# Kernel optimization log

Hardware: AMD Instinct MI355X
Metric: run time of the kernel (lower is better)

The kernel has to match this reference:

```python
import jax, jax.numpy as jnp
import numpy as np

D, T, B = 128, 64, 512
EPS = 1e-5


def setup_inputs() -> dict:
    key = jax.random.key(0)
    k1, k2, k3, k4, k5 = jax.random.split(key, 5)
    inp = jax.random.normal(k1, (D, T, B), jnp.float32) * 0.1
    returns_partition = jax.random.normal(k2, (D, T, B), jnp.float32) * 0.01
    target = jax.random.normal(k3, (D,), jnp.float32) * 0.1
    hidden = jnp.zeros((D, 1, B), jnp.float32)  # forward arg (overwritten at t=0)
    # diagonally-dominant weight so the per-row denominators v[j,j] stay away from 0
    W = jnp.eye(D, dtype=jnp.float32) + 0.1 * jax.random.normal(k4, (D, D), jnp.float32)
    b = 0.1 * jax.random.normal(k5, (D,), jnp.float32)
    return {"input": inp, "target": target, "returns_partition": returns_partition,
            "hidden": hidden, "W": W, "b": b}


def _recurrence(h, v, absb, pi_bar):
    # h, pi_bar: [D, B]; v: [D, D] (row-normalized); absb: [D]
    d = h.shape[0]
    vd = jnp.diagonal(v)                                  # v[j, j], torch.matmul(vj, e_j)
    s = v @ (h - pi_bar)                                  # [D, B], s[j] = vj . (h - pi_bar)
    lam_p = (absb[:, None] - s) / vd[:, None]
    lam_m = (-absb[:, None] - s) / vd[:, None]
    delta = (jnp.where(s > absb[:, None], lam_p, 0.0)
             + jnp.where(s < -absb[:, None], lam_m, 0.0))  # [D, B]
    # hidden_new_j = h + delta[j] * e_j  =>  v @ (hidden_new_j - pi_bar) = s + v[:, j] (x) delta[j]
    snew = s[None, :, :] + v.T[:, :, None] * delta[:, None, :]      # [J, D, B]
    inside = (snew < absb[None, :, None] + EPS) & (snew > -absb[None, :, None] - EPS)
    # torch: judge_mat[j] = min over rows; then max over j  == any_j(all_k(...))
    judge_mat = jnp.any(jnp.all(inside, axis=1), axis=0).astype(h.dtype)  # [B]

    # sequential per-coordinate projection (order matters: row j uses updated state)
    def body(ht, j):
        sj = v[j] @ (ht - pi_bar)                          # [B]
        lp = (absb[j] - sj) / v[j, j]
        lm = (-absb[j] - sj) / v[j, j]
        dj = jnp.where(sj > absb[j], lp, 0.0) + jnp.where(sj < -absb[j], lm, 0.0)
        return ht.at[j].add(dj), None
    h_temp, _ = jax.lax.scan(body, h, jnp.arange(d))

    # 10-step bisection between pi_bar (feasible) and (1 - judge_mat) * h
    def bis(carry, _):
        h_in, h_out = carry
        h_m = h_in + (h_out - h_in) * 0.5
        sm = v @ (h_m - pi_bar)
        j = jnp.all((sm <= absb[:, None] + EPS) & (sm >= -absb[:, None] - EPS), axis=0)  # [B]
        return (jnp.where(j, h_m, h_in), jnp.where(j, h_out, h_m)), h_m
    h_out0 = (1.0 - judge_mat) * h
    _, h_ms = jax.lax.scan(bis, (pi_bar, h_out0), None, length=10)
    h_m = h_ms[-1]
    return judge_mat * h_temp + (1.0 - judge_mat) * h_m


def reference(input, target, returns_partition, hidden, W, b):
    d, t, bsz = input.shape
    norm = jnp.linalg.norm(W, axis=1, keepdims=True)
    v = W / jnp.maximum(norm, 1e-12)                      # F.normalize(W, p=2, dim=1)
    absb = jnp.abs(b)
    pi_bar = jnp.broadcast_to(target[:, None], (d, bsz))  # [D, B]

    h0 = input[:, 0, :]                                   # t = 0: hidden := input slice
    rs = jnp.moveaxis(returns_partition[:, :t - 1, :], 1, 0)  # [T-1, D, B]

    def step(h, r):
        adj = h * (1.0 + r) / (1.0 + jnp.sum(h * r, axis=0))
        hn = _recurrence(adj, v, absb, pi_bar)
        return hn, hn

    h_last, hs = jax.lax.scan(step, h0, rs)
    output = jnp.concatenate([h0[:, None, :], jnp.moveaxis(hs, 0, 1)], axis=1)  # [D, T, B]
    return output, h_last[:, None, :]
```

## Files before the change

kernel.cpp:

```cpp
#include <hip/hip_runtime.h>
#include <cstdint>

#define D 128
#define T 64
#define B 512
#define EPSF 1e-5f

__device__ __forceinline__ float lane_bcast(float x, int l) {
    return __int_as_float(__builtin_amdgcn_readlane(__float_as_int(x), l));
}

__device__ __forceinline__ float2 colpair(const float* csh, int j, int i2) {
    int f2 = j * 64 + (i2 ^ ((j & 7) << 1));
    return *(const float2*)(csh + 2 * f2);
}

__global__ __launch_bounds__(64) void prep_kernel(const float* __restrict__ W,
                                                  const float* __restrict__ b,
                                                  float* __restrict__ csw,
                                                  float* __restrict__ vd,
                                                  float* __restrict__ absb) {
    const int i = blockIdx.x;
    const int l = threadIdx.x;
    float w0 = W[i * D + l];
    float w1 = W[i * D + l + 64];
    float p = w0 * w0 + w1 * w1;
#pragma unroll
    for (int off = 32; off; off >>= 1) p += __shfl_xor(p, off);
    float norm = sqrtf(p);
    float scale = norm > 1e-12f ? norm : 1e-12f;
    float v0 = w0 / scale;
    float v1 = w1 / scale;
    const int i2 = i & 63, half = i >> 6;
    const int sw = (l & 7) << 1;
    csw[2 * (l * 64 + (i2 ^ sw)) + half] = v0;
    csw[2 * ((l + 64) * 64 + (i2 ^ sw)) + half] = v1;
    if (i < 64) { if (l == i) vd[i] = v0; }
    else        { if (l == i - 64) vd[i] = v1; }
    if (i == 0) {
        absb[l] = fabsf(b[l]);
        absb[l + 64] = fabsf(b[l + 64]);
    }
}

__global__ __launch_bounds__(128, 1) void rnn_kernel(const float* __restrict__ input,
                                                     const float* __restrict__ target,
                                                     const float* __restrict__ returns,
                                                     const float* __restrict__ W,
                                                     const float* __restrict__ cswg,
                                                     const float* __restrict__ vdg,
                                                     const float* __restrict__ absbg,
                                                     float* __restrict__ out) {
    __shared__ float csh[D * D];
    __shared__ float s_sh[2][2 * 64];
    __shared__ float ae_sh[2 * 64];

    const int tid = threadIdx.x;
    const int w = tid >> 6;
    const int lane = tid & 63;
    const int b = blockIdx.x * 2 + w;
    const int rlo = lane, rhi = lane + 64;

    {
        const float4* src = (const float4*)cswg;
        float4* dst = (float4*)csh;
#pragma unroll
        for (int c = 0; c < 32; ++c) dst[c * 128 + tid] = src[c * 128 + tid];
    }

    const float tgt_lo = target[rlo], tgt_hi = target[rhi];
    const float a_lo = absbg[rlo], a_hi = absbg[rhi];
    const float aeps_lo = a_lo + EPSF, aeps_hi = a_hi + EPSF;
    const float vd_lo = vdg[rlo], vd_hi = vdg[rhi];
    const float rvd_lo = 1.0f / vd_lo, rvd_hi = 1.0f / vd_hi;

    if (w == 0) *(float2*)&ae_sh[2 * lane] = make_float2(aeps_lo, aeps_hi);

    float4 va4[32], vb4[32];
    {
        const float4* wa = (const float4*)(W + rlo * D);
        const float4* wb = (const float4*)(W + rhi * D);
        float na0 = 0, na1 = 0, na2 = 0, na3 = 0;
        float nb0 = 0, nb1 = 0, nb2 = 0, nb3 = 0;
#pragma unroll
        for (int c = 0; c < 32; ++c) {
            float4 A = wa[c], Bv = wb[c];
            va4[c] = A; vb4[c] = Bv;
            na0 = fmaf(A.x, A.x, na0); na1 = fmaf(A.y, A.y, na1);
            na2 = fmaf(A.z, A.z, na2); na3 = fmaf(A.w, A.w, na3);
            nb0 = fmaf(Bv.x, Bv.x, nb0); nb1 = fmaf(Bv.y, Bv.y, nb1);
            nb2 = fmaf(Bv.z, Bv.z, nb2); nb3 = fmaf(Bv.w, Bv.w, nb3);
        }
        float nna = sqrtf((na0 + na1) + (na2 + na3));
        float nnb = sqrtf((nb0 + nb1) + (nb2 + nb3));
        float ra = 1.0f / (nna > 1e-12f ? nna : 1e-12f);
        float rb = 1.0f / (nnb > 1e-12f ? nnb : 1e-12f);
#pragma unroll
        for (int c = 0; c < 32; ++c) {
            va4[c].x *= ra; va4[c].y *= ra; va4[c].z *= ra; va4[c].w *= ra;
            vb4[c].x *= rb; vb4[c].y *= rb; vb4[c].z *= rb; vb4[c].w *= rb;
        }
    }
    __syncthreads();

    const float* va = (const float*)va4;
    const float* vb = (const float*)vb4;

    float h_lo = input[rlo * T * B + b];
    float h_hi = input[rhi * T * B + b];
    out[rlo * T * B + b] = h_lo;
    out[rhi * T * B + b] = h_hi;

    float r_lo = returns[rlo * T * B + b];
    float r_hi = returns[rhi * T * B + b];

    for (int t = 1; t < T; ++t) {
        float num_lo = h_lo * (1.0f + r_lo);
        float num_hi = h_hi * (1.0f + r_hi);
        float p = h_lo * r_lo + h_hi * r_hi;
#pragma unroll
        for (int off = 32; off; off >>= 1) p += __shfl_xor(p, off);
        float den = 1.0f + p;
        float adj_lo = num_lo / den;
        float adj_hi = num_hi / den;

        if (t < T - 1) {
            r_lo = returns[rlo * T * B + t * B + b];
            r_hi = returns[rhi * T * B + t * B + b];
        }

        const float x_lo = adj_lo - tgt_lo;
        const float x_hi = adj_hi - tgt_hi;

        float a0 = 0, a1 = 0, a2 = 0, a3 = 0;
        float b0 = 0, b1 = 0, b2 = 0, b3 = 0;
#pragma unroll
        for (int k = 0; k < 128; ++k) {
            float xk = (k < 64) ? lane_bcast(x_lo, k) : lane_bcast(x_hi, k - 64);
            switch (k & 3) {
                case 0: a0 = fmaf(va[k], xk, a0); b0 = fmaf(vb[k], xk, b0); break;
                case 1: a1 = fmaf(va[k], xk, a1); b1 = fmaf(vb[k], xk, b1); break;
                case 2: a2 = fmaf(va[k], xk, a2); b2 = fmaf(vb[k], xk, b2); break;
                default: a3 = fmaf(va[k], xk, a3); b3 = fmaf(vb[k], xk, b3); break;
            }
        }
        float s_lo = (a0 + a1) + (a2 + a3);
        float s_hi = (b0 + b1) + (b2 + b3);

        h_lo = adj_lo;
        h_hi = adj_hi;

        bool viol_lo = (s_lo > a_lo) || (s_lo < -a_lo);
        bool viol_hi = (s_hi > a_hi) || (s_hi < -a_hi);
        uint64_t mlo = __ballot(viol_lo);
        uint64_t mhi = __ballot(viol_hi);

        if ((mlo | mhi) != 0ull) {
            float dl = 0.0f, dh = 0.0f;
            if (s_lo > a_lo) dl = (a_lo - s_lo) / vd_lo;
            else if (s_lo < -a_lo) dl = (-a_lo - s_lo) / vd_lo;
            if (s_hi > a_hi) dh = (a_hi - s_hi) / vd_hi;
            else if (s_hi < -a_hi) dh = (-a_hi - s_hi) / vd_hi;

            int V = __popcll(mlo) + __popcll(mhi);
            bool judge = false;

            if (V <= 8) {
                bool in_lo = (s_lo < aeps_lo) && (s_lo > -aeps_lo);
                bool in_hi = (s_hi < aeps_hi) && (s_hi > -aeps_hi);
                judge = (__ballot(in_lo && in_hi) == ~0ull);
                if (!judge) {
                    uint64_t tml = mlo, tmh = mhi;
                    int jn[8];
                    float djs[8];
                    float2 cps[8];
#pragma unroll
                    for (int q = 0; q < 8; ++q) {
                        int j = -1;
                        if (tml) {
                            j = (int)__ffsll((unsigned long long)tml) - 1;
                            tml &= tml - 1;
                        } else if (tmh) {
                            j = 64 + (int)__ffsll((unsigned long long)tmh) - 1;
                            tmh &= tmh - 1;
                        }
                        jn[q] = j;
                        if (j >= 0) {
                            djs[q] = lane_bcast((j < 64) ? dl : dh, j & 63);
                            cps[q] = colpair(csh, j, lane);
                        }
                    }
#pragma unroll
                    for (int q = 0; q < 8; ++q) {
                        if (jn[q] >= 0 && !judge) {
                            float n_lo = fmaf(cps[q].x, djs[q], s_lo);
                            float n_hi = fmaf(cps[q].y, djs[q], s_hi);
                            bool pl = (n_lo < aeps_lo) && (n_lo > -aeps_lo);
                            bool ph = (n_hi < aeps_hi) && (n_hi > -aeps_hi);
                            if (__ballot(pl && ph) == ~0ull) judge = true;
                        }
                    }
                }
            } else {
                *(float2*)&s_sh[w][2 * lane] = make_float2(s_lo, s_hi);
                float m1 = -1.0f, m2 = -1.0f;
#pragma unroll
                for (int c = 0; c < 32; ++c) {
                    int f4 = lane * 32 + (c ^ (lane & 7));
                    float4 c1 = *(const float4*)(csh + 4 * f4);
                    float4 c2 = *(const float4*)(csh + 4 * f4 + 8192);
                    float4 sv = *(const float4*)&s_sh[w][4 * c];
                    float4 ae = *(const float4*)&ae_sh[4 * c];
                    m1 = fmaxf(m1, fabsf(fmaf(c1.x, dl, sv.x)) - ae.x);
                    m1 = fmaxf(m1, fabsf(fmaf(c1.y, dl, sv.y)) - ae.y);
                    m1 = fmaxf(m1, fabsf(fmaf(c1.z, dl, sv.z)) - ae.z);
                    m1 = fmaxf(m1, fabsf(fmaf(c1.w, dl, sv.w)) - ae.w);
                    m2 = fmaxf(m2, fabsf(fmaf(c2.x, dh, sv.x)) - ae.x);
                    m2 = fmaxf(m2, fabsf(fmaf(c2.y, dh, sv.y)) - ae.y);
                    m2 = fmaxf(m2, fabsf(fmaf(c2.z, dh, sv.z)) - ae.z);
                    m2 = fmaxf(m2, fabsf(fmaf(c2.w, dh, sv.w)) - ae.w);
                }
                judge = ((__ballot(m1 < 0.0f) | __ballot(m2 < 0.0f)) != 0ull);
            }

            if (judge) {
                uint64_t rem_lo = ~0ull, rem_hi = ~0ull;
                while (true) {
                    uint64_t m1b = __ballot((s_lo > a_lo) || (s_lo < -a_lo)) & rem_lo;
                    uint64_t m2b = __ballot((s_hi > a_hi) || (s_hi < -a_hi)) & rem_hi;
                    int j;
                    if (m1b) {
                        int jl = (int)__ffsll((unsigned long long)m1b) - 1;
                        j = jl;
                        rem_lo = (jl == 63) ? 0ull : (~0ull << (jl + 1));
                    } else if (m2b) {
                        int jh = (int)__ffsll((unsigned long long)m2b) - 1;
                        j = 64 + jh;
                        rem_lo = 0ull;
                        rem_hi = (jh == 63) ? 0ull : (~0ull << (jh + 1));
                    } else {
                        break;
                    }
                    float dl2 = (s_lo > a_lo) ? (a_lo - s_lo) * rvd_lo
                               : ((s_lo < -a_lo) ? (-a_lo - s_lo) * rvd_lo : 0.0f);
                    float dh2 = (s_hi > a_hi) ? (a_hi - s_hi) * rvd_hi
                               : ((s_hi < -a_hi) ? (-a_hi - s_hi) * rvd_hi : 0.0f);
                    float srcv = (j < 64) ? dl2 : dh2;
                    float dj = lane_bcast(srcv, j & 63);
                    if (lane == (j & 63)) {
                        if (j < 64) h_lo += dj; else h_hi += dj;
                    }
                    float2 cp = colpair(csh, j, lane);
                    s_lo = fmaf(cp.x, dj, s_lo);
                    s_hi = fmaf(cp.y, dj, s_hi);
                }
            } else {
                float hin_lo = tgt_lo, hin_hi = tgt_hi;
                float sin_lo = 0.0f, sin_hi = 0.0f;
                float hout_lo = h_lo, hout_hi = h_hi;
                float sout_lo = s_lo, sout_hi = s_hi;
                float hm_lo = 0.0f, hm_hi = 0.0f;
#pragma unroll
                for (int it = 0; it < 10; ++it) {
                    hm_lo = hin_lo + (hout_lo - hin_lo) * 0.5f;
                    hm_hi = hin_hi + (hout_hi - hin_hi) * 0.5f;
                    float sm_lo = sin_lo + (sout_lo - sin_lo) * 0.5f;
                    float sm_hi = sin_hi + (sout_hi - sin_hi) * 0.5f;
                    bool pl = (sm_lo <= aeps_lo) && (sm_lo >= -aeps_lo);
                    bool ph = (sm_hi <= aeps_hi) && (sm_hi >= -aeps_hi);
                    bool inside = (__ballot(pl && ph) == ~0ull);
                    if (inside) {
                        hin_lo = hm_lo; hin_hi = hm_hi;
                        sin_lo = sm_lo; sin_hi = sm_hi;
                    } else {
                        hout_lo = hm_lo; hout_hi = hm_hi;
                        sout_lo = sm_lo; sout_hi = sm_hi;
                    }
                }
                h_lo = hm_lo;
                h_hi = hm_hi;
            }
        }

        out[rlo * T * B + t * B + b] = h_lo;
        out[rhi * T * B + t * B + b] = h_hi;
    }

    out[D * T * B + rlo * B + b] = h_lo;
    out[D * T * B + rhi * B + b] = h_hi;
}

extern "C" void kernel_launch(void* const* d_in, const int* in_sizes, int n_in,
                              void* d_out, int out_size, void* d_ws, size_t ws_size,
                              hipStream_t stream) {
    const float* input   = (const float*)d_in[0];
    const float* target  = (const float*)d_in[1];
    const float* returns = (const float*)d_in[2];
    const float* W = (const float*)d_in[4];
    const float* b = (const float*)d_in[5];
    float* out = (float*)d_out;

    float* csw  = (float*)d_ws;
    float* vd   = csw + D * D;
    float* absb = vd + D;

    prep_kernel<<<D, 64, 0, stream>>>(W, b, csw, vd, absb);
    rnn_kernel<<<B / 2, 128, 0, stream>>>(input, target, returns, W, csw, vd, absb, out);
}
```

Measured before the change: 239.5 us.

## Read weight columns from LDS instead of registers and batch projection lookahead

The per-thread register copy of the normalized weight rows (256 floats per thread) is dropped, and the mat-vec now streams swizzled column pairs from shared memory. The launch-bounds minimum-occupancy hint is removed, so register pressure falls and occupancy can rise. The sequential projection loop now prefetches up to four violating column pairs per pass and validates each against the live violation mask, aborting the batch when order changes. The swizzle indexing for the s/eps vectors in the judge check is also adjusted. In exchange, every mat-vec step pays an extra LDS read, and the projection loop gains branching complexity.

```diff
diff --git a/kernel.cpp b/kernel.cpp
--- a/kernel.cpp
+++ b/kernel.cpp
@@ -43,14 +43,13 @@
     }
 }
 
-__global__ __launch_bounds__(128, 1) void rnn_kernel(const float* __restrict__ input,
-                                                     const float* __restrict__ target,
-                                                     const float* __restrict__ returns,
-                                                     const float* __restrict__ W,
-                                                     const float* __restrict__ cswg,
-                                                     const float* __restrict__ vdg,
-                                                     const float* __restrict__ absbg,
-                                                     float* __restrict__ out) {
+__global__ __launch_bounds__(128) void rnn_kernel(const float* __restrict__ input,
+                                                  const float* __restrict__ target,
+                                                  const float* __restrict__ returns,
+                                                  const float* __restrict__ cswg,
+                                                  const float* __restrict__ vdg,
+                                                  const float* __restrict__ absbg,
+                                                  float* __restrict__ out) {
     __shared__ float csh[D * D];
     __shared__ float s_sh[2][2 * 64];
     __shared__ float ae_sh[2 * 64];
@@ -75,36 +74,12 @@
     const float rvd_lo = 1.0f / vd_lo, rvd_hi = 1.0f / vd_hi;
 
     if (w == 0) *(float2*)&ae_sh[2 * lane] = make_float2(aeps_lo, aeps_hi);
-
-    float4 va4[32], vb4[32];
-    {
-        const float4* wa = (const float4*)(W + rlo * D);
-        const float4* wb = (const float4*)(W + rhi * D);
-        float na0 = 0, na1 = 0, na2 = 0, na3 = 0;
-        float nb0 = 0, nb1 = 0, nb2 = 0, nb3 = 0;
-#pragma unroll
-        for (int c = 0; c < 32; ++c) {
-            float4 A = wa[c], Bv = wb[c];
-            va4[c] = A; vb4[c] = Bv;
-            na0 = fmaf(A.x, A.x, na0); na1 = fmaf(A.y, A.y, na1);
-            na2 = fmaf(A.z, A.z, na2); na3 = fmaf(A.w, A.w, na3);
-            nb0 = fmaf(Bv.x, Bv.x, nb0); nb1 = fmaf(Bv.y, Bv.y, nb1);
-            nb2 = fmaf(Bv.z, Bv.z, nb2); nb3 = fmaf(Bv.w, Bv.w, nb3);
-        }
-        float nna = sqrtf((na0 + na1) + (na2 + na3));
-        float nnb = sqrtf((nb0 + nb1) + (nb2 + nb3));
-        float ra = 1.0f / (nna > 1e-12f ? nna : 1e-12f);
-        float rb = 1.0f / (nnb > 1e-12f ? nnb : 1e-12f);
-#pragma unroll
-        for (int c = 0; c < 32; ++c) {
-            va4[c].x *= ra; va4[c].y *= ra; va4[c].z *= ra; va4[c].w *= ra;
-            vb4[c].x *= rb; vb4[c].y *= rb; vb4[c].z *= rb; vb4[c].w *= rb;
-        }
-    }
     __syncthreads();
 
-    const float* va = (const float*)va4;
-    const float* vb = (const float*)vb4;
+    const char* colp[8];
+#pragma unroll
+    for (int c = 0; c < 8; ++c)
+        colp[c] = (const char*)csh + 8 * (lane ^ (c << 1));
 
     float h_lo = input[rlo * T * B + b];
     float h_hi = input[rhi * T * B + b];
@@ -136,12 +111,13 @@
         float b0 = 0, b1 = 0, b2 = 0, b3 = 0;
 #pragma unroll
         for (int k = 0; k < 128; ++k) {
-            float xk = (k < 64) ? lane_bcast(x_lo, k) : lane_bcast(x_hi, k - 64);
+            float2 cp = *(const float2*)(colp[k & 7] + k * 512);
+            float xk = lane_bcast((k < 64) ? x_lo : x_hi, k & 63);
             switch (k & 3) {
-                case 0: a0 = fmaf(va[k], xk, a0); b0 = fmaf(vb[k], xk, b0); break;
-                case 1: a1 = fmaf(va[k], xk, a1); b1 = fmaf(vb[k], xk, b1); break;
-                case 2: a2 = fmaf(va[k], xk, a2); b2 = fmaf(vb[k], xk, b2); break;
-                default: a3 = fmaf(va[k], xk, a3); b3 = fmaf(vb[k], xk, b3); break;
+                case 0: a0 = fmaf(cp.x, xk, a0); b0 = fmaf(cp.y, xk, b0); break;
+                case 1: a1 = fmaf(cp.x, xk, a1); b1 = fmaf(cp.y, xk, b1); break;
+                case 2: a2 = fmaf(cp.x, xk, a2); b2 = fmaf(cp.y, xk, b2); break;
+                default: a3 = fmaf(cp.x, xk, a3); b3 = fmaf(cp.y, xk, b3); break;
             }
         }
         float s_lo = (a0 + a1) + (a2 + a3);
@@ -150,10 +126,8 @@
         h_lo = adj_lo;
         h_hi = adj_hi;
 
-        bool viol_lo = (s_lo > a_lo) || (s_lo < -a_lo);
-        bool viol_hi = (s_hi > a_hi) || (s_hi < -a_hi);
-        uint64_t mlo = __ballot(viol_lo);
-        uint64_t mhi = __ballot(viol_hi);
+        uint64_t mlo = __ballot(fabsf(s_lo) > a_lo);
+        uint64_t mhi = __ballot(fabsf(s_hi) > a_hi);
 
         if ((mlo | mhi) != 0ull) {
             float dl = 0.0f, dh = 0.0f;
@@ -209,8 +183,9 @@
                     int f4 = lane * 32 + (c ^ (lane & 7));
                     float4 c1 = *(const float4*)(csh + 4 * f4);
                     float4 c2 = *(const float4*)(csh + 4 * f4 + 8192);
-                    float4 sv = *(const float4*)&s_sh[w][4 * c];
-                    float4 ae = *(const float4*)&ae_sh[4 * c];
+                    int i2a = (2 * c) ^ ((lane & 7) << 1);
+                    float4 sv = *(const float4*)&s_sh[w][2 * i2a];
+                    float4 ae = *(const float4*)&ae_sh[2 * i2a];
                     m1 = fmaxf(m1, fabsf(fmaf(c1.x, dl, sv.x)) - ae.x);
                     m1 = fmaxf(m1, fabsf(fmaf(c1.y, dl, sv.y)) - ae.y);
                     m1 = fmaxf(m1, fabsf(fmaf(c1.z, dl, sv.z)) - ae.z);
@@ -226,33 +201,58 @@
             if (judge) {
                 uint64_t rem_lo = ~0ull, rem_hi = ~0ull;
                 while (true) {
-                    uint64_t m1b = __ballot((s_lo > a_lo) || (s_lo < -a_lo)) & rem_lo;
-                    uint64_t m2b = __ballot((s_hi > a_hi) || (s_hi < -a_hi)) & rem_hi;
-                    int j;
-                    if (m1b) {
-                        int jl = (int)__ffsll((unsigned long long)m1b) - 1;
-                        j = jl;
-                        rem_lo = (jl == 63) ? 0ull : (~0ull << (jl + 1));
-                    } else if (m2b) {
-                        int jh = (int)__ffsll((unsigned long long)m2b) - 1;
-                        j = 64 + jh;
-                        rem_lo = 0ull;
-                        rem_hi = (jh == 63) ? 0ull : (~0ull << (jh + 1));
-                    } else {
-                        break;
-                    }
-                    float dl2 = (s_lo > a_lo) ? (a_lo - s_lo) * rvd_lo
-                               : ((s_lo < -a_lo) ? (-a_lo - s_lo) * rvd_lo : 0.0f);
-                    float dh2 = (s_hi > a_hi) ? (a_hi - s_hi) * rvd_hi
-                               : ((s_hi < -a_hi) ? (-a_hi - s_hi) * rvd_hi : 0.0f);
-                    float srcv = (j < 64) ? dl2 : dh2;
-                    float dj = lane_bcast(srcv, j & 63);
-                    if (lane == (j & 63)) {
-                        if (j < 64) h_lo += dj; else h_hi += dj;
-                    }
-                    float2 cp = colpair(csh, j, lane);
-                    s_lo = fmaf(cp.x, dj, s_lo);
-                    s_hi = fmaf(cp.y, dj, s_hi);
+                    uint64_t vl = __ballot(fabsf(s_lo) > a_lo) & rem_lo;
+                    uint64_t vh = __ballot(fabsf(s_hi) > a_hi) & rem_hi;
+                    if (!(vl | vh)) break;
+                    int jq[4];
+                    float2 cpq[4];
+                    {
+                        uint64_t tl = vl, th = vh;
+#pragma unroll
+                        for (int q = 0; q < 4; ++q) {
+                            int j = -1;
+                            if (tl) {
+                                j = (int)__ffsll((unsigned long long)tl) - 1;
+                                tl &= tl - 1;
+                            } else if (th) {
+                                j = 64 + (int)__ffsll((unsigned long long)th) - 1;
+                                th &= th - 1;
+                            }
+                            jq[q] = j;
+                            if (j >= 0) cpq[q] = colpair(csh, j, lane);
+                        }
+                    }
+                    bool abort = false;
+#pragma unroll
+                    for (int q = 0; q < 4; ++q) {
+                        if (abort || jq[q] < 0) continue;
+                        uint64_t cl = __ballot(fabsf(s_lo) > a_lo) & rem_lo;
+                        uint64_t ch = __ballot(fabsf(s_hi) > a_hi) & rem_hi;
+                        int jl = cl ? (int)__ffsll((unsigned long long)cl) - 1
+                                    : (ch ? 64 + (int)__ffsll((unsigned long long)ch) - 1 : -1);
+                        if (jl < 0) { rem_lo = rem_hi = 0ull; abort = true; continue; }
+                        if (jl < jq[q]) { abort = true; continue; }
+                        if (jl > jq[q]) continue;
+                        float tl2 = (s_lo > a_lo) ? (a_lo - s_lo)
+                                   : ((s_lo < -a_lo) ? (-a_lo - s_lo) : 0.0f);
+                        float th2 = (s_hi > a_hi) ? (a_hi - s_hi)
+                                   : ((s_hi < -a_hi) ? (-a_hi - s_hi) : 0.0f);
+                        float dj = lane_bcast((jq[q] < 64) ? tl2 * rvd_lo : th2 * rvd_hi,
+                                              jq[q] & 63);
+                        if (lane == (jq[q] & 63)) {
+                            if (jq[q] < 64) h_lo += dj; else h_hi += dj;
+                        }
+                        s_lo = fmaf(cpq[q].x, dj, s_lo);
+                        s_hi = fmaf(cpq[q].y, dj, s_hi);
+                        if (jq[q] < 64) {
+                            rem_lo = (jq[q] == 63) ? 0ull : (~0ull << (jq[q] + 1));
+                        } else {
+                            rem_lo = 0ull;
+                            int sh = jq[q] - 64;
+                            rem_hi = (sh == 63) ? 0ull : (~0ull << (sh + 1));
+                        }
+                    }
+                    if (!(rem_lo | rem_hi)) break;
                 }
             } else {
                 float hin_lo = tgt_lo, hin_hi = tgt_hi;
@@ -305,5 +305,5 @@
     float* absb = vd + D;
 
     prep_kernel<<<D, 64, 0, stream>>>(W, b, csw, vd, absb);
-    rnn_kernel<<<B / 2, 128, 0, stream>>>(input, target, returns, W, csw, vd, absb, out);
-}
+    rnn_kernel<<<B / 2, 128, 0, stream>>>(input, target, returns, csw, vd, absb, out);
+}
```

Result: no change. 235.5 us (-1.7%).

## Read normalized weights from LDS instead of per-thread registers in matvec

Applied to the files above, without the earlier changes.

Drops the 256-float per-thread register copy of the normalized weight rows. The matvec now reads float4 quads from a new swizzled interleaved shared-memory layout that packs column pairs for the lo and hi rows together. This cuts VGPR pressure and lets more than one block run per CU, since the launch bound no longer forces occupancy 1. It also caches the small-violation column pairs for reuse in the sequential projection loop and replaces serial ballots with a shuffle reduction of a bitmask. The cost is extra LDS traffic on every timestep's matvec.

```diff
diff --git a/kernel.cpp b/kernel.cpp
--- a/kernel.cpp
+++ b/kernel.cpp
@@ -8,11 +8,6 @@
 
 __device__ __forceinline__ float lane_bcast(float x, int l) {
     return __int_as_float(__builtin_amdgcn_readlane(__float_as_int(x), l));
-}
-
-__device__ __forceinline__ float2 colpair(const float* csh, int j, int i2) {
-    int f2 = j * 64 + (i2 ^ ((j & 7) << 1));
-    return *(const float2*)(csh + 2 * f2);
 }
 
 __global__ __launch_bounds__(64) void prep_kernel(const float* __restrict__ W,
@@ -32,9 +27,10 @@
     float v0 = w0 / scale;
     float v1 = w1 / scale;
     const int i2 = i & 63, half = i >> 6;
-    const int sw = (l & 7) << 1;
-    csw[2 * (l * 64 + (i2 ^ sw)) + half] = v0;
-    csw[2 * ((l + 64) * 64 + (i2 ^ sw)) + half] = v1;
+    const int j2 = l >> 1, par = l & 1;
+    const int sub = par + 2 * half;
+    csw[4 * (j2 * 64 + (i2 ^ (j2 & 7))) + sub] = v0;
+    csw[4 * ((32 + j2) * 64 + (i2 ^ (j2 & 7))) + sub] = v1;
     if (i < 64) { if (l == i) vd[i] = v0; }
     else        { if (l == i - 64) vd[i] = v1; }
     if (i == 0) {
@@ -43,14 +39,19 @@
     }
 }
 
-__global__ __launch_bounds__(128, 1) void rnn_kernel(const float* __restrict__ input,
-                                                     const float* __restrict__ target,
-                                                     const float* __restrict__ returns,
-                                                     const float* __restrict__ W,
-                                                     const float* __restrict__ cswg,
-                                                     const float* __restrict__ vdg,
-                                                     const float* __restrict__ absbg,
-                                                     float* __restrict__ out) {
+__device__ __forceinline__ float2 colq(const float* csh, int j, int i2) {
+    int j2 = j >> 1;
+    const float4 q = *(const float4*)(csh + 4 * (j2 * 64 + (i2 ^ (j2 & 7))));
+    return (j & 1) ? make_float2(q.y, q.w) : make_float2(q.x, q.z);
+}
+
+__global__ __launch_bounds__(128) void rnn_kernel(const float* __restrict__ input,
+                                                  const float* __restrict__ target,
+                                                  const float* __restrict__ returns,
+                                                  const float* __restrict__ cswg,
+                                                  const float* __restrict__ vdg,
+                                                  const float* __restrict__ absbg,
+                                                  float* __restrict__ out) {
     __shared__ float csh[D * D];
     __shared__ float s_sh[2][2 * 64];
     __shared__ float ae_sh[2 * 64];
@@ -75,36 +76,11 @@
     const float rvd_lo = 1.0f / vd_lo, rvd_hi = 1.0f / vd_hi;
 
     if (w == 0) *(float2*)&ae_sh[2 * lane] = make_float2(aeps_lo, aeps_hi);
-
-    float4 va4[32], vb4[32];
-    {
-        const float4* wa = (const float4*)(W + rlo * D);
-        const float4* wb = (const float4*)(W + rhi * D);
-        float na0 = 0, na1 = 0, na2 = 0, na3 = 0;
-        float nb0 = 0, nb1 = 0, nb2 = 0, nb3 = 0;
-#pragma unroll
-        for (int c = 0; c < 32; ++c) {
-            float4 A = wa[c], Bv = wb[c];
-            va4[c] = A; vb4[c] = Bv;
-            na0 = fmaf(A.x, A.x, na0); na1 = fmaf(A.y, A.y, na1);
-            na2 = fmaf(A.z, A.z, na2); na3 = fmaf(A.w, A.w, na3);
-            nb0 = fmaf(Bv.x, Bv.x, nb0); nb1 = fmaf(Bv.y, Bv.y, nb1);
-            nb2 = fmaf(Bv.z, Bv.z, nb2); nb3 = fmaf(Bv.w, Bv.w, nb3);
-        }
-        float nna = sqrtf((na0 + na1) + (na2 + na3));
-        float nnb = sqrtf((nb0 + nb1) + (nb2 + nb3));
-        float ra = 1.0f / (nna > 1e-12f ? nna : 1e-12f);
-        float rb = 1.0f / (nnb > 1e-12f ? nnb : 1e-12f);
-#pragma unroll
-        for (int c = 0; c < 32; ++c) {
-            va4[c].x *= ra; va4[c].y *= ra; va4[c].z *= ra; va4[c].w *= ra;
-            vb4[c].x *= rb; vb4[c].y *= rb; vb4[c].z *= rb; vb4[c].w *= rb;
-        }
-    }
     __syncthreads();
 
-    const float* va = (const float*)va4;
-    const float* vb = (const float*)vb4;
+    const char* qb[8];
+#pragma unroll
+    for (int c = 0; c < 8; ++c) qb[c] = (const char*)csh + 16 * (lane ^ c);
 
     float h_lo = input[rlo * T * B + b];
     float h_hi = input[rhi * T * B + b];
@@ -132,28 +108,31 @@
         const float x_lo = adj_lo - tgt_lo;
         const float x_hi = adj_hi - tgt_hi;
 
-        float a0 = 0, a1 = 0, a2 = 0, a3 = 0;
-        float b0 = 0, b1 = 0, b2 = 0, b3 = 0;
-#pragma unroll
-        for (int k = 0; k < 128; ++k) {
-            float xk = (k < 64) ? lane_bcast(x_lo, k) : lane_bcast(x_hi, k - 64);
-            switch (k & 3) {
-                case 0: a0 = fmaf(va[k], xk, a0); b0 = fmaf(vb[k], xk, b0); break;
-                case 1: a1 = fmaf(va[k], xk, a1); b1 = fmaf(vb[k], xk, b1); break;
-                case 2: a2 = fmaf(va[k], xk, a2); b2 = fmaf(vb[k], xk, b2); break;
-                default: a3 = fmaf(va[k], xk, a3); b3 = fmaf(vb[k], xk, b3); break;
+        float a0 = 0, a1 = 0, b0 = 0, b1 = 0;
+#pragma unroll
+        for (int j2 = 0; j2 < 64; ++j2) {
+            float4 q = *(const float4*)(qb[j2 & 7] + j2 * 1024);
+            float x0, x1;
+            if (j2 < 32) {
+                x0 = lane_bcast(x_lo, 2 * j2);
+                x1 = lane_bcast(x_lo, 2 * j2 + 1);
+            } else {
+                x0 = lane_bcast(x_hi, 2 * j2 - 64);
+                x1 = lane_bcast(x_hi, 2 * j2 - 63);
             }
+            a0 = fmaf(q.x, x0, a0);
+            a1 = fmaf(q.y, x1, a1);
+            b0 = fmaf(q.z, x0, b0);
+            b1 = fmaf(q.w, x1, b1);
         }
-        float s_lo = (a0 + a1) + (a2 + a3);
-        float s_hi = (b0 + b1) + (b2 + b3);
+        float s_lo = a0 + a1;
+        float s_hi = b0 + b1;
 
         h_lo = adj_lo;
         h_hi = adj_hi;
 
-        bool viol_lo = (s_lo > a_lo) || (s_lo < -a_lo);
-        bool viol_hi = (s_hi > a_hi) || (s_hi < -a_hi);
-        uint64_t mlo = __ballot(viol_lo);
-        uint64_t mhi = __ballot(viol_hi);
+        uint64_t mlo = __ballot(fabsf(s_lo) > a_lo);
+        uint64_t mhi = __ballot(fabsf(s_hi) > a_hi);
 
         if ((mlo | mhi) != 0ull) {
             float dl = 0.0f, dh = 0.0f;
@@ -165,15 +144,17 @@
             int V = __popcll(mlo) + __popcll(mhi);
             bool judge = false;
 
+            int jn[8];
+            float djs[8], clo_q[8], chi_q[8];
+#pragma unroll
+            for (int q = 0; q < 8; ++q) { jn[q] = -1; djs[q] = 0; clo_q[q] = 0; chi_q[q] = 0; }
+
             if (V <= 8) {
                 bool in_lo = (s_lo < aeps_lo) && (s_lo > -aeps_lo);
                 bool in_hi = (s_hi < aeps_hi) && (s_hi > -aeps_hi);
                 judge = (__ballot(in_lo && in_hi) == ~0ull);
-                if (!judge) {
+                {
                     uint64_t tml = mlo, tmh = mhi;
-                    int jn[8];
-                    float djs[8];
-                    float2 cps[8];
 #pragma unroll
                     for (int q = 0; q < 8; ++q) {
                         int j = -1;
@@ -187,38 +168,51 @@
                         jn[q] = j;
                         if (j >= 0) {
                             djs[q] = lane_bcast((j < 64) ? dl : dh, j & 63);
-                            cps[q] = colpair(csh, j, lane);
+                            float2 cp = colq(csh, j, lane);
+                            clo_q[q] = cp.x;
+                            chi_q[q] = cp.y;
                         }
                     }
+                }
+                if (!judge) {
+                    unsigned mbits = 0;
 #pragma unroll
                     for (int q = 0; q < 8; ++q) {
-                        if (jn[q] >= 0 && !judge) {
-                            float n_lo = fmaf(cps[q].x, djs[q], s_lo);
-                            float n_hi = fmaf(cps[q].y, djs[q], s_hi);
-                            bool pl = (n_lo < aeps_lo) && (n_lo > -aeps_lo);
-                            bool ph = (n_hi < aeps_hi) && (n_hi > -aeps_hi);
-                            if (__ballot(pl && ph) == ~0ull) judge = true;
+                        if (jn[q] >= 0) {
+                            float n_lo = fmaf(clo_q[q], djs[q], s_lo);
+                            float n_hi = fmaf(chi_q[q], djs[q], s_hi);
+                            bool ok = (n_lo < aeps_lo) && (n_lo > -aeps_lo) &&
+                                      (n_hi < aeps_hi) && (n_hi > -aeps_hi);
+                            mbits |= ok ? (1u << q) : 0u;
                         }
                     }
+#pragma unroll
+                    for (int off = 1; off < 64; off <<= 1)
+                        mbits &= (unsigned)__shfl_xor((int)mbits, off);
+                    judge = (mbits != 0u);
                 }
             } else {
                 *(float2*)&s_sh[w][2 * lane] = make_float2(s_lo, s_hi);
+                const int par = lane & 1;
+                const int j2s = lane >> 1;
+                const float* jbase = csh + 4 * (j2s * 64);
+                const int jx = j2s & 7;
                 float m1 = -1.0f, m2 = -1.0f;
 #pragma unroll
-                for (int c = 0; c < 32; ++c) {
-                    int f4 = lane * 32 + (c ^ (lane & 7));
-                    float4 c1 = *(const float4*)(csh + 4 * f4);
-                    float4 c2 = *(const float4*)(csh + 4 * f4 + 8192);
-                    float4 sv = *(const float4*)&s_sh[w][4 * c];
-                    float4 ae = *(const float4*)&ae_sh[4 * c];
-                    m1 = fmaxf(m1, fabsf(fmaf(c1.x, dl, sv.x)) - ae.x);
-                    m1 = fmaxf(m1, fabsf(fmaf(c1.y, dl, sv.y)) - ae.y);
-                    m1 = fmaxf(m1, fabsf(fmaf(c1.z, dl, sv.z)) - ae.z);
-                    m1 = fmaxf(m1, fabsf(fmaf(c1.w, dl, sv.w)) - ae.w);
-                    m2 = fmaxf(m2, fabsf(fmaf(c2.x, dh, sv.x)) - ae.x);
-                    m2 = fmaxf(m2, fabsf(fmaf(c2.y, dh, sv.y)) - ae.y);
-                    m2 = fmaxf(m2, fabsf(fmaf(c2.z, dh, sv.z)) - ae.z);
-                    m2 = fmaxf(m2, fabsf(fmaf(c2.w, dh, sv.w)) - ae.w);
+                for (int c = 0; c < 64; ++c) {
+                    const float* pr = jbase + 4 * (c ^ jx);
+                    float4 q1 = *(const float4*)pr;
+                    float4 q2 = *(const float4*)(pr + 8192);
+                    float c1lo = par ? q1.y : q1.x;
+                    float c1hi = par ? q1.w : q1.z;
+                    float c2lo = par ? q2.y : q2.x;
+                    float c2hi = par ? q2.w : q2.z;
+                    float2 sv = *(const float2*)&s_sh[w][2 * c];
+                    float2 ae = *(const float2*)&ae_sh[2 * c];
+                    m1 = fmaxf(m1, fabsf(fmaf(c1lo, dl, sv.x)) - ae.x);
+                    m1 = fmaxf(m1, fabsf(fmaf(c1hi, dl, sv.y)) - ae.y);
+                    m2 = fmaxf(m2, fabsf(fmaf(c2lo, dh, sv.x)) - ae.x);
+                    m2 = fmaxf(m2, fabsf(fmaf(c2hi, dh, sv.y)) - ae.y);
                 }
                 judge = ((__ballot(m1 < 0.0f) | __ballot(m2 < 0.0f)) != 0ull);
             }
@@ -226,8 +220,8 @@
             if (judge) {
                 uint64_t rem_lo = ~0ull, rem_hi = ~0ull;
                 while (true) {
-                    uint64_t m1b = __ballot((s_lo > a_lo) || (s_lo < -a_lo)) & rem_lo;
-                    uint64_t m2b = __ballot((s_hi > a_hi) || (s_hi < -a_hi)) & rem_hi;
+                    uint64_t m1b = __ballot(fabsf(s_lo) > a_lo) & rem_lo;
+                    uint64_t m2b = __ballot(fabsf(s_hi) > a_hi) & rem_hi;
                     int j;
                     if (m1b) {
                         int jl = (int)__ffsll((unsigned long long)m1b) - 1;
@@ -245,14 +239,21 @@
                                : ((s_lo < -a_lo) ? (-a_lo - s_lo) * rvd_lo : 0.0f);
                     float dh2 = (s_hi > a_hi) ? (a_hi - s_hi) * rvd_hi
                                : ((s_hi < -a_hi) ? (-a_hi - s_hi) * rvd_hi : 0.0f);
-                    float srcv = (j < 64) ? dl2 : dh2;
-                    float dj = lane_bcast(srcv, j & 63);
+                    float dj = lane_bcast((j < 64) ? dl2 : dh2, j & 63);
                     if (lane == (j & 63)) {
                         if (j < 64) h_lo += dj; else h_hi += dj;
                     }
-                    float2 cp = colpair(csh, j, lane);
-                    s_lo = fmaf(cp.x, dj, s_lo);
-                    s_hi = fmaf(cp.y, dj, s_hi);
+                    float clo = 0.0f, chi = 0.0f;
+                    bool have = false;
+#pragma unroll
+                    for (int q = 0; q < 8; ++q)
+                        if (jn[q] == j) { clo = clo_q[q]; chi = chi_q[q]; have = true; }
+                    if (!have) {
+                        float2 cp = colq(csh, j, lane);
+                        clo = cp.x; chi = cp.y;
+                    }
+                    s_lo = fmaf(clo, dj, s_lo);
+                    s_hi = fmaf(chi, dj, s_hi);
                 }
             } else {
                 float hin_lo = tgt_lo, hin_hi = tgt_hi;
@@ -305,5 +306,5 @@
     float* absb = vd + D;
 
     prep_kernel<<<D, 64, 0, stream>>>(W, b, csw, vd, absb);
-    rnn_kernel<<<B / 2, 128, 0, stream>>>(input, target, returns, W, csw, vd, absb, out);
-}
+    rnn_kernel<<<B / 2, 128, 0, stream>>>(input, target, returns, csw, vd, absb, out);
+}
```

Result: slower. 250.1 us (+4.4%).
